# Kernel tuning notes

Measured on AMD Instinct MI355X. Metric: run time of the kernel, lower is better.

The kernel has to match this reference:

```python
import jax, jax.numpy as jnp
import numpy as np

EMB_SIZE = 768
BLOCK_SIZE = 64
OFFSET = 1  # bert cls offset


def setup_inputs() -> dict:
    key = jax.random.key(0)
    ks = jax.random.split(key, 10)
    n, c, d, h, E, M, P = 4, 1024, 768, 12, 42, 8, 1024
    sequence_output = jax.random.normal(ks[0], (n, c, d), jnp.float32)
    attention = jax.random.uniform(ks[1], (n, h, c, c), jnp.float32)
    attention = attention / attention.sum(-1, keepdims=True)  # softmax-like rows
    Wh = jax.random.normal(ks[2], (EMB_SIZE, 2 * d), jnp.float32) * 0.02
    bh = jax.random.normal(ks[3], (EMB_SIZE,), jnp.float32) * 0.02
    Wt = jax.random.normal(ks[4], (EMB_SIZE, 2 * d), jnp.float32) * 0.02
    bt = jax.random.normal(ks[5], (EMB_SIZE,), jnp.float32) * 0.02
    Wb = jax.random.normal(ks[6], (99, EMB_SIZE * BLOCK_SIZE), jnp.float32) * 0.02
    mention_pos = jax.random.randint(ks[7], (n, E, M), 0, c - 1 - OFFSET, jnp.int32)
    mention_mask = jax.random.randint(ks[8], (n, E, M), 0, 2, jnp.int32)
    mention_mask = mention_mask.at[:, :, 0].set(1)  # every entity has >=1 mention
    hts = jax.random.randint(ks[9], (n, P, 2), 0, E, jnp.int32)
    return {"sequence_output": sequence_output, "attention": attention,
            "Wh": Wh, "bh": bh, "Wt": Wt, "bt": bt, "Wb": Wb,
            "mention_pos": mention_pos, "mention_mask": mention_mask, "hts": hts}


def _get_hrt_doc(seq, att, pos, mask, ht):
    # seq [c,d], att [h,c,c], pos/mask [E,M], ht [P,2]
    p = pos + OFFSET                                   # [E,M]
    valid = mask > 0
    memb = seq[p]                                      # [E,M,d] gather
    e_emb = jax.scipy.special.logsumexp(
        jnp.where(valid[..., None], memb, -jnp.inf), axis=1)  # [E,d]
    matt = att[:, p]                                   # [h,E,M,c] gather
    cnt = valid.sum(1).astype(seq.dtype)               # [E]
    e_att = (matt * valid[None, :, :, None].astype(seq.dtype)).sum(2)
    e_att = jnp.transpose(e_att, (1, 0, 2)) / cnt[:, None, None]  # [E,h,c] mention mean
    hs = e_emb[ht[:, 0]]                               # [P,d]
    ts = e_emb[ht[:, 1]]
    h_att = e_att[ht[:, 0]]                            # [P,h,c]
    t_att = e_att[ht[:, 1]]
    ht_att = (h_att * t_att).mean(1)                   # [P,c] head mean
    ht_att = ht_att / (ht_att.sum(1, keepdims=True) + 1e-5)
    rs = jnp.einsum('ld,rl->rd', seq, ht_att)          # [P,d]
    return hs, ts, rs


def reference(sequence_output, attention, Wh, bh, Wt, bt, Wb,
              mention_pos, mention_mask, hts):
    d = sequence_output.shape[-1]
    hs, ts, rs = jax.vmap(_get_hrt_doc)(sequence_output, attention,
                                        mention_pos, mention_mask, hts)
    hs = hs.reshape(-1, d)
    ts = ts.reshape(-1, d)
    rs = rs.reshape(-1, d)
    hs = jnp.tanh(jnp.concatenate([hs, rs], axis=1) @ Wh.T + bh)
    ts = jnp.tanh(jnp.concatenate([ts, rs], axis=1) @ Wt.T + bt)
    nb = EMB_SIZE // BLOCK_SIZE
    b1 = hs.reshape(-1, nb, BLOCK_SIZE)
    b2 = ts.reshape(-1, nb, BLOCK_SIZE)
    bl = (b1[:, :, :, None] * b2[:, :, None, :]).reshape(-1, EMB_SIZE * BLOCK_SIZE)
    logits = bl @ Wb.T                                 # [N, num_labels+2]
    return logits
```

## Files before the change

### kernel.cpp

```cpp
#include <hip/hip_runtime.h>
#include <hip/hip_bf16.h>
#include <hip/hip_fp16.h>
#include <math.h>

#define NDOC 4
#define CCC  1024
#define DDD  768
#define HHH  12
#define EEE  42
#define MMM  8
#define PPP  1024
#define NBQ  12
#define NK   99
#define NPAD 112

typedef __attribute__((ext_vector_type(8))) short short8v;
typedef __attribute__((ext_vector_type(8))) _Float16 half8;
typedef __attribute__((ext_vector_type(4))) float floatx4;

__device__ __forceinline__ unsigned short f32_to_bf16u(float f) {
  return __builtin_bit_cast(unsigned short, __float2bfloat16(f));
}
__device__ __forceinline__ unsigned short f32_to_f16u(float f) {
  return __builtin_bit_cast(unsigned short, __float2half(f));
}

__global__ __launch_bounds__(256) void k_eemb(const float* __restrict__ seq,
    const int* __restrict__ pos, const int* __restrict__ mask,
    unsigned short* __restrict__ eembB) {
  int e = blockIdx.x, doc = blockIdx.y;
  int base = (doc*EEE + e)*MMM;
  int p[MMM], mk[MMM];
#pragma unroll
  for (int m = 0; m < MMM; ++m) { p[m] = pos[base+m] + 1; mk[m] = mask[base+m]; }
  for (int d0 = threadIdx.x; d0 < DDD; d0 += 256) {
    float v[MMM]; float mx = -INFINITY;
#pragma unroll
    for (int m = 0; m < MMM; ++m) {
      v[m] = seq[(doc*CCC + p[m])*DDD + d0];
      if (mk[m]) mx = fmaxf(mx, v[m]);
    }
    float s = 0.f;
#pragma unroll
    for (int m = 0; m < MMM; ++m) if (mk[m]) s += expf(v[m]-mx);
    eembB[(doc*EEE + e)*DDD + d0] = f32_to_bf16u(logf(s) + mx);
  }
}

__global__ __launch_bounds__(256) void k_eatt(const float* __restrict__ att,
    const int* __restrict__ pos, const int* __restrict__ mask,
    float* __restrict__ eatt) {
  int head = blockIdx.x, e = blockIdx.y, doc = blockIdx.z;
  int base = (doc*EEE + e)*MMM;
  int j = threadIdx.x * 4;
  float ax=0.f, ay=0.f, az=0.f, aw=0.f; float cnt = 0.f;
#pragma unroll
  for (int m = 0; m < MMM; ++m) {
    int mk = mask[base+m];
    cnt += (float)mk;
    if (mk) {
      int pp = pos[base+m] + 1;
      const float4 a = *(const float4*)&att[((size_t)(doc*HHH + head)*CCC + pp)*CCC + j];
      ax += a.x; ay += a.y; az += a.z; aw += a.w;
    }
  }
  float inv = 1.f / cnt;
  float4 o; o.x = ax*inv; o.y = ay*inv; o.z = az*inv; o.w = aw*inv;
  *(float4*)&eatt[((size_t)((doc*EEE + e)*HHH + head))*CCC + j] = o;
}

__global__ __launch_bounds__(256) void k_htatt(const float* __restrict__ eatt,
    const int* __restrict__ hts, unsigned short* __restrict__ htB) {
  int b = blockIdx.x; int doc = b >> 10; int r = b & 1023;
  int h0 = hts[(doc*PPP + r)*2 + 0];
  int t0 = hts[(doc*PPP + r)*2 + 1];
  const float* ea0 = &eatt[(size_t)((doc*EEE + h0)*HHH)*CCC];
  const float* ea1 = &eatt[(size_t)((doc*EEE + t0)*HHH)*CCC];
  int j = threadIdx.x * 4;
  float vx=0.f, vy=0.f, vz=0.f, vw=0.f;
#pragma unroll
  for (int hh = 0; hh < HHH; ++hh) {
    const float4 a  = *(const float4*)&ea0[hh*CCC + j];
    const float4 bq = *(const float4*)&ea1[hh*CCC + j];
    vx += a.x*bq.x; vy += a.y*bq.y; vz += a.z*bq.z; vw += a.w*bq.w;
  }
  const float inv12 = 1.f/12.f;
  vx *= inv12; vy *= inv12; vz *= inv12; vw *= inv12;
  float part = vx + vy + vz + vw;
  __shared__ float red[4];
  for (int off = 32; off > 0; off >>= 1) part += __shfl_down(part, off, 64);
  int lane = threadIdx.x & 63, wv = threadIdx.x >> 6;
  if (lane == 0) red[wv] = part;
  __syncthreads();
  if (threadIdx.x == 0) red[0] = red[0]+red[1]+red[2]+red[3];
  __syncthreads();
  float sc = 1.f / (red[0] + 1e-5f);
  unsigned short o[4];
  o[0] = f32_to_bf16u(vx*sc); o[1] = f32_to_bf16u(vy*sc);
  o[2] = f32_to_bf16u(vz*sc); o[3] = f32_to_bf16u(vw*sc);
  *(uint2*)&htB[((size_t)(doc*PPP + r))*CCC + j] = *(const uint2*)o;
}

__global__ __launch_bounds__(256) void k_packW(const float* __restrict__ Wh,
    const float* __restrict__ Wt, unsigned short* __restrict__ WB) {
  int gid = blockIdx.x*256 + threadIdx.x;
  int half = gid >= 147456;
  int loc = half ? gid - 147456 : gid;
  const float* src = (half ? Wt : Wh) + (size_t)loc*8;
  float4 v0 = *(const float4*)src;
  float4 v1 = *(const float4*)(src+4);
  unsigned short o[8];
  o[0]=f32_to_bf16u(v0.x); o[1]=f32_to_bf16u(v0.y); o[2]=f32_to_bf16u(v0.z); o[3]=f32_to_bf16u(v0.w);
  o[4]=f32_to_bf16u(v1.x); o[5]=f32_to_bf16u(v1.y); o[6]=f32_to_bf16u(v1.z); o[7]=f32_to_bf16u(v1.w);
  *(uint4*)&WB[(size_t)half*1179648 + (size_t)loc*8] = *(const uint4*)o;
}

__global__ __launch_bounds__(256) void k_seqT(const float* __restrict__ seq,
    unsigned short* __restrict__ seqTB) {
  __shared__ float tl[64][65];
  int d0 = blockIdx.x * 64, c0 = blockIdx.y * 64, doc = blockIdx.z;
  int t = threadIdx.x;
#pragma unroll
  for (int rep = 0; rep < 4; ++rep) {
    int cr = rep*16 + (t >> 4);
    int d4 = (t & 15) * 4;
    float4 v = *(const float4*)&seq[((size_t)doc*CCC + c0 + cr)*DDD + d0 + d4];
    tl[cr][d4+0]=v.x; tl[cr][d4+1]=v.y; tl[cr][d4+2]=v.z; tl[cr][d4+3]=v.w;
  }
  __syncthreads();
#pragma unroll
  for (int rep = 0; rep < 4; ++rep) {
    int dr = rep*16 + (t >> 4);
    int c4 = (t & 15) * 4;
    unsigned short o[4];
#pragma unroll
    for (int kq = 0; kq < 4; ++kq)
      o[kq] = f32_to_bf16u(tl[c4+kq][dr]);
    *(uint2*)&seqTB[((size_t)doc*DDD + d0 + dr)*CCC + c0 + c4] = *(const uint2*)o;
  }
}

__global__ __launch_bounds__(256) void k_rs_mfma(
    const unsigned short* __restrict__ htB,
    const unsigned short* __restrict__ seqTB,
    unsigned short* __restrict__ rsB) {
  __shared__ unsigned short A_l[4096];
  __shared__ unsigned short B_l[4096];
  const int n0 = blockIdx.x * 128;
  const int m0 = blockIdx.y * 128;
  const int doc = m0 >> 10;
  const int mloc = m0 & 1023;
  const int t = threadIdx.x;
  const int lane = t & 63;
  const int ln = lane & 15, q4 = lane >> 4;
  const int w = t >> 6;
  const int wr = w >> 1, wc = w & 1;

  const int r0 = t >> 2;
  const int koff = (t & 3) * 8;
  const unsigned short* srcA0 = htB + ((size_t)doc*CCC + mloc + r0)*CCC + koff;
  const unsigned short* srcA1 = htB + ((size_t)doc*CCC + mloc + r0 + 64)*CCC + koff;
  const unsigned short* srcB0 = seqTB + ((size_t)doc*DDD + n0 + r0)*CCC + koff;
  const unsigned short* srcB1 = seqTB + ((size_t)doc*DDD + n0 + r0 + 64)*CCC + koff;

  floatx4 acc[4][4];
#pragma unroll
  for (int i = 0; i < 4; ++i)
#pragma unroll
    for (int j = 0; j < 4; ++j) acc[i][j] = (floatx4){0.f,0.f,0.f,0.f};

  for (int k0 = 0; k0 < CCC; k0 += 32) {
    uint4 va0 = *(const uint4*)(srcA0 + k0);
    uint4 va1 = *(const uint4*)(srcA1 + k0);
    uint4 vb0 = *(const uint4*)(srcB0 + k0);
    uint4 vb1 = *(const uint4*)(srcB1 + k0);
    __syncthreads();
    *(uint4*)&A_l[(size_t)t*8]       = va0;
    *(uint4*)&A_l[(size_t)(t+256)*8] = va1;
    *(uint4*)&B_l[(size_t)t*8]       = vb0;
    *(uint4*)&B_l[(size_t)(t+256)*8] = vb1;
    __syncthreads();
    short8v a[4], b[4];
#pragma unroll
    for (int rt = 0; rt < 4; ++rt)
      a[rt] = *(const short8v*)&A_l[((wr*64 + rt*16 + ln)*4 + q4)*8];
#pragma unroll
    for (int nt = 0; nt < 4; ++nt)
      b[nt] = *(const short8v*)&B_l[((wc*64 + nt*16 + ln)*4 + q4)*8];
#pragma unroll
    for (int rt = 0; rt < 4; ++rt)
#pragma unroll
      for (int nt = 0; nt < 4; ++nt)
        acc[rt][nt] = __builtin_amdgcn_mfma_f32_16x16x32_bf16(a[rt], b[nt], acc[rt][nt], 0, 0, 0);
  }
#pragma unroll
  for (int rt = 0; rt < 4; ++rt)
#pragma unroll
    for (int nt = 0; nt < 4; ++nt) {
      int col = n0 + wc*64 + nt*16 + ln;
#pragma unroll
      for (int reg = 0; reg < 4; ++reg) {
        int row = m0 + wr*64 + rt*16 + q4*4 + reg;
        rsB[(size_t)row*DDD + col] = f32_to_bf16u(acc[rt][nt][reg]);
      }
    }
}

__global__ __launch_bounds__(256) void k_heads_mfma(
    const unsigned short* __restrict__ eembB,
    const unsigned short* __restrict__ rsB,
    const int* __restrict__ hts,
    const unsigned short* __restrict__ WB,
    const float* __restrict__ bh, const float* __restrict__ bt,
    float* __restrict__ hsb, float* __restrict__ tsb) {
  __shared__ unsigned short A_l[4096];
  __shared__ unsigned short B_l[4096];
  const int which = blockIdx.z;
  const int n0 = blockIdx.x * 128;
  const int m0 = blockIdx.y * 128;
  const int doc = m0 >> 10;
  const int t = threadIdx.x;
  const int lane = t & 63;
  const int ln = lane & 15, q4 = lane >> 4;
  const int w = t >> 6;
  const int wr = w >> 1, wc = w & 1;

  const int r0 = t >> 2;
  const int koff = (t & 3) * 8;
  const int rgA0 = m0 + r0, rgA1 = m0 + r0 + 64;
  const int idx0 = hts[rgA0*2 + which];
  const int idx1 = hts[rgA1*2 + which];
  const unsigned short* srcE0 = eembB + (size_t)(doc*EEE + idx0)*DDD + koff;
  const unsigned short* srcE1 = eembB + (size_t)(doc*EEE + idx1)*DDD + koff;
  const unsigned short* srcR0 = rsB + (size_t)rgA0*DDD + koff;
  const unsigned short* srcR1 = rsB + (size_t)rgA1*DDD + koff;
  const unsigned short* WBz = WB + (size_t)which*1179648;
  const unsigned short* srcW0 = WBz + (size_t)(n0 + r0)*1536 + koff;
  const unsigned short* srcW1 = WBz + (size_t)(n0 + r0 + 64)*1536 + koff;

  floatx4 acc[4][4];
#pragma unroll
  for (int i = 0; i < 4; ++i)
#pragma unroll
    for (int j = 0; j < 4; ++j) acc[i][j] = (floatx4){0.f,0.f,0.f,0.f};

  for (int k0 = 0; k0 < 1536; k0 += 32) {
    uint4 va0 = (k0 < DDD) ? *(const uint4*)(srcE0 + k0) : *(const uint4*)(srcR0 + (k0 - DDD));
    uint4 va1 = (k0 < DDD) ? *(const uint4*)(srcE1 + k0) : *(const uint4*)(srcR1 + (k0 - DDD));
    uint4 vb0 = *(const uint4*)(srcW0 + k0);
    uint4 vb1 = *(const uint4*)(srcW1 + k0);
    __syncthreads();
    *(uint4*)&A_l[(size_t)t*8]       = va0;
    *(uint4*)&A_l[(size_t)(t+256)*8] = va1;
    *(uint4*)&B_l[(size_t)t*8]       = vb0;
    *(uint4*)&B_l[(size_t)(t+256)*8] = vb1;
    __syncthreads();
    short8v a[4], b[4];
#pragma unroll
    for (int rt = 0; rt < 4; ++rt)
      a[rt] = *(const short8v*)&A_l[((wr*64 + rt*16 + ln)*4 + q4)*8];
#pragma unroll
    for (int nt = 0; nt < 4; ++nt)
      b[nt] = *(const short8v*)&B_l[((wc*64 + nt*16 + ln)*4 + q4)*8];
#pragma unroll
    for (int rt = 0; rt < 4; ++rt)
#pragma unroll
      for (int nt = 0; nt < 4; ++nt)
        acc[rt][nt] = __builtin_amdgcn_mfma_f32_16x16x32_bf16(a[rt], b[nt], acc[rt][nt], 0, 0, 0);
  }
  const float* bias = which ? bt : bh;
  float* outp = which ? tsb : hsb;
#pragma unroll
  for (int rt = 0; rt < 4; ++rt)
#pragma unroll
    for (int nt = 0; nt < 4; ++nt) {
      int col = n0 + wc*64 + nt*16 + ln;
      float bsv = bias[col];
#pragma unroll
      for (int reg = 0; reg < 4; ++reg) {
        int row = m0 + wr*64 + rt*16 + q4*4 + reg;
        outp[(size_t)row*DDD + col] = tanhf(acc[rt][nt][reg] + bsv);
      }
    }
}

__global__ __launch_bounds__(256) void k_prep_w(const float* __restrict__ Wb,
    unsigned short* __restrict__ Wp) {
  int t = blockIdx.x*256 + threadIdx.x;
  int j = (t & 7) * 8;
  int n = (t >> 3) % NPAD;
  int ki = t / 896;
  unsigned short o[8];
  if (n < NK) {
    const float* src = &Wb[(size_t)n*49152 + ki*64 + j];
    float4 v0 = *(const float4*)src;
    float4 v1 = *(const float4*)(src+4);
    o[0]=f32_to_f16u(v0.x); o[1]=f32_to_f16u(v0.y); o[2]=f32_to_f16u(v0.z); o[3]=f32_to_f16u(v0.w);
    o[4]=f32_to_f16u(v1.x); o[5]=f32_to_f16u(v1.y); o[6]=f32_to_f16u(v1.z); o[7]=f32_to_f16u(v1.w);
  } else {
#pragma unroll
    for (int e=0;e<8;++e) o[e]=0;
  }
  *(uint4*)&Wp[(size_t)ki*7168 + n*64 + j] = *(const uint4*)o;
}

__global__ __launch_bounds__(256) void k_pack_hs(const float* __restrict__ hs,
    unsigned short* __restrict__ hsT) {
  __shared__ float tl[64][65];
  int i0 = blockIdx.x * 64, r0 = blockIdx.y * 64;
  int t = threadIdx.x;
#pragma unroll
  for (int rep = 0; rep < 4; ++rep) {
    int r = rep*16 + (t >> 4);
    int c4 = (t & 15) * 4;
    float4 v = *(const float4*)&hs[(size_t)(r0 + r)*DDD + i0 + c4];
    tl[r][c4+0]=v.x; tl[r][c4+1]=v.y; tl[r][c4+2]=v.z; tl[r][c4+3]=v.w;
  }
  __syncthreads();
#pragma unroll
  for (int rep = 0; rep < 4; ++rep) {
    int i = rep*16 + (t >> 4);
    int r4 = (t & 15) * 4;
    unsigned short o[4];
#pragma unroll
    for (int kq = 0; kq < 4; ++kq)
      o[kq] = f32_to_f16u(tl[r4+kq][i]);
    *(uint2*)&hsT[(size_t)(i0 + i)*4096 + r0 + r4] = *(const uint2*)o;
  }
}

__global__ __launch_bounds__(256, 3) void k_logits_mfma(
    const unsigned short* __restrict__ hsT,
    const float* __restrict__ tsb,
    const unsigned short* __restrict__ Wp,
    unsigned short* __restrict__ P) {
  __shared__ unsigned short hsT_l[32*128];
  __shared__ unsigned short Bt_l[2*NPAD*72];
  const int slice = blockIdx.x;
  const int kbase = (slice >> 1)*64 + (slice & 1)*32;
  const int mtile = blockIdx.y;
  const int t = threadIdx.x;
  const int w = t >> 6;
  const int lane = t & 63;
  const int ln = lane & 15;
  const int q = lane >> 4;
  const int m0w = mtile*128 + w*32;

#pragma unroll
  for (int rep = 0; rep < 2; ++rep) {
    int c16 = t + rep*256;
    int ii = c16 >> 4;
    int c8 = (c16 & 15) * 8;
    uint4 v = *(const uint4*)&hsT[(size_t)(kbase + ii)*4096 + mtile*128 + c8];
    *(uint4*)&hsT_l[ii*128 + c8] = v;
  }

  __half2 tsr2[2][2][4];
#pragma unroll
  for (int rt = 0; rt < 2; ++rt) {
    int row = m0w + rt*16 + ln;
    int nb = kbase >> 6;
#pragma unroll
    for (int js = 0; js < 2; ++js) {
      const float* p = &tsb[(size_t)row*DDD + nb*64 + js*32 + q*8];
      float4 v0 = *(const float4*)p;
      float4 v1 = *(const float4*)(p+4);
      tsr2[rt][js][0] = __floats2half2_rn(v0.x, v0.y);
      tsr2[rt][js][1] = __floats2half2_rn(v0.z, v0.w);
      tsr2[rt][js][2] = __floats2half2_rn(v1.x, v1.y);
      tsr2[rt][js][3] = __floats2half2_rn(v1.z, v1.w);
    }
  }

  floatx4 acc[2][7];
#pragma unroll
  for (int rt = 0; rt < 2; ++rt)
#pragma unroll
    for (int nt = 0; nt < 7; ++nt)
      acc[rt][nt] = (floatx4){0.f,0.f,0.f,0.f};

  uint4 wreg[4];
#pragma unroll
  for (int r = 0; r < 4; ++r) {
    int chunk = t + r*256;
    if (chunk < 896) wreg[r] = *(const uint4*)&Wp[(size_t)kbase*7168 + chunk*8];
  }
#pragma unroll
  for (int r = 0; r < 4; ++r) {
    int chunk = t + r*256;
    if (chunk < 896) {
      int n = chunk >> 3, j8 = (chunk & 7)*8;
      *(uint4*)&Bt_l[n*72 + j8] = wreg[r];
    }
  }
  __syncthreads();

  for (int ii = 0; ii < 32; ++ii) {
    const unsigned short* bufc = Bt_l + (ii & 1)*(NPAD*72);
    if (ii < 31) {
      int ki = kbase + ii + 1;
#pragma unroll
      for (int r = 0; r < 4; ++r) {
        int chunk = t + r*256;
        if (chunk < 896) wreg[r] = *(const uint4*)&Wp[(size_t)ki*7168 + chunk*8];
      }
    }
    __half2 hh[2];
#pragma unroll
    for (int rt = 0; rt < 2; ++rt) {
      unsigned short hb = hsT_l[ii*128 + w*32 + rt*16 + ln];
      hh[rt] = __half2half2(__ushort_as_half(hb));
    }
#pragma unroll
    for (int js = 0; js < 2; ++js) {
      half8 a[2];
#pragma unroll
      for (int rt = 0; rt < 2; ++rt) {
        uint4 au;
        au.x = __builtin_bit_cast(unsigned int, __hmul2(hh[rt], tsr2[rt][js][0]));
        au.y = __builtin_bit_cast(unsigned int, __hmul2(hh[rt], tsr2[rt][js][1]));
        au.z = __builtin_bit_cast(unsigned int, __hmul2(hh[rt], tsr2[rt][js][2]));
        au.w = __builtin_bit_cast(unsigned int, __hmul2(hh[rt], tsr2[rt][js][3]));
        a[rt] = __builtin_bit_cast(half8, au);
      }
#pragma unroll
      for (int nt = 0; nt < 7; ++nt) {
        half8 b = __builtin_bit_cast(half8,
            *(const short8v*)&bufc[(nt*16 + ln)*72 + js*32 + q*8]);
#pragma unroll
        for (int rt = 0; rt < 2; ++rt)
          acc[rt][nt] = __builtin_amdgcn_mfma_f32_16x16x32_f16(a[rt], b, acc[rt][nt], 0, 0, 0);
      }
    }
    if (ii < 31) {
      __syncthreads();
#pragma unroll
      for (int r = 0; r < 4; ++r) {
        int chunk = t + r*256;
        if (chunk < 896) {
          int n = chunk >> 3, j8 = (chunk & 7)*8;
          *(uint4*)&Bt_l[((ii+1) & 1)*(NPAD*72) + n*72 + j8] = wreg[r];
        }
      }
      __syncthreads();
    }
  }

  unsigned short* Ps = P + (size_t)slice*(4096*NPAD);
#pragma unroll
  for (int nt = 0; nt < 7; ++nt) {
    int col = nt*16 + ln;
#pragma unroll
    for (int rt = 0; rt < 2; ++rt) {
#pragma unroll
      for (int reg = 0; reg < 4; ++reg) {
        int row = m0w + rt*16 + q*4 + reg;
        Ps[(size_t)row*NPAD + col] = f32_to_f16u(acc[rt][nt][reg]);
      }
    }
  }
}

__global__ __launch_bounds__(256) void k_logred(const unsigned short* __restrict__ P,
    float* __restrict__ out) {
  int idx = blockIdx.x*256 + threadIdx.x;
  int r = idx / NPAD;
  int c = idx % NPAD;
  if (c >= NK) return;
  float s = 0.f;
#pragma unroll
  for (int sl = 0; sl < 24; ++sl)
    s += __half2float(__ushort_as_half(P[(size_t)sl*(4096*NPAD) + idx]));
  out[(size_t)r*NK + c] = s;
}

extern "C" void kernel_launch(void* const* d_in, const int* in_sizes, int n_in,
                              void* d_out, int out_size, void* d_ws, size_t ws_size,
                              hipStream_t stream) {
  const float* seq  = (const float*)d_in[0];
  const float* att  = (const float*)d_in[1];
  const float* Wh   = (const float*)d_in[2];
  const float* bh   = (const float*)d_in[3];
  const float* Wt   = (const float*)d_in[4];
  const float* bt   = (const float*)d_in[5];
  const float* Wb   = (const float*)d_in[6];
  const int* pos    = (const int*)d_in[7];
  const int* mask   = (const int*)d_in[8];
  const int* hts    = (const int*)d_in[9];
  float* out = (float*)d_out;

  float* ws = (float*)d_ws;
  float*          eatt  = ws;
  unsigned short* htB   = (unsigned short*)(ws + 2064384);
  unsigned short* eembB = (unsigned short*)(ws + 4161536);
  unsigned short* seqTB = (unsigned short*)(ws + 4226048);
  unsigned short* WhtB  = (unsigned short*)(ws + 5798912);
  unsigned short* rsB   = (unsigned short*)(ws + 6978560);
  float*          hsb   = ws + 8551424;
  float*          tsb   = ws + 11697152;
  unsigned short* WpB   = (unsigned short*)eatt;
  unsigned short* hsTB  = (unsigned short*)seqTB;
  unsigned short* Pp    = (unsigned short*)(ws + 5798912);

  k_eemb<<<dim3(EEE, NDOC), 256, 0, stream>>>(seq, pos, mask, eembB);
  k_eatt<<<dim3(HHH, EEE, NDOC), 256, 0, stream>>>(att, pos, mask, eatt);
  k_htatt<<<dim3(NDOC*PPP), 256, 0, stream>>>(eatt, hts, htB);
  k_packW<<<dim3(1152), 256, 0, stream>>>(Wh, Wt, WhtB);
  k_seqT<<<dim3(DDD/64, CCC/64, NDOC), 256, 0, stream>>>(seq, seqTB);
  k_rs_mfma<<<dim3(6, 32), 256, 0, stream>>>(htB, seqTB, rsB);
  k_prep_w<<<dim3(2688), 256, 0, stream>>>(Wb, WpB);
  k_heads_mfma<<<dim3(6, 32, 2), 256, 0, stream>>>(eembB, rsB, hts, WhtB, bh, bt, hsb, tsb);
  k_pack_hs<<<dim3(DDD/64, 4096/64), 256, 0, stream>>>(hsb, hsTB);
  k_logits_mfma<<<dim3(24, 32), 256, 0, stream>>>(hsTB, tsb, WpB, Pp);
  k_logred<<<dim3(4096*NPAD/256), 256, 0, stream>>>(Pp, out);
}
```

Before: 226.5 us.

## Pre-swizzle Wb into MFMA fragment order and double per-warp row tile in logits kernel

The Wb prep kernel now writes fp16 weights in the exact lane order of the MFMA B-fragment, so the logits kernel can copy them linearly into LDS and read each fragment with a contiguous lane*8 load instead of a padded strided layout. The logits kernel also drops to 128 threads per block, with each warp covering 64 rows (4 row tiles) instead of 32, so each B fragment feeds twice as many MFMAs. This cuts LDS traffic and address math per MFMA, at the cost of more accumulator registers per thread and fewer warps per block to hide latency.

```diff
diff --git a/kernel.cpp b/kernel.cpp
--- a/kernel.cpp
+++ b/kernel.cpp
@@ -287,12 +287,12 @@
 __global__ __launch_bounds__(256) void k_prep_w(const float* __restrict__ Wb,
     unsigned short* __restrict__ Wp) {
   int t = blockIdx.x*256 + threadIdx.x;
-  int j = (t & 7) * 8;
+  int j8 = (t & 7) * 8;
   int n = (t >> 3) % NPAD;
   int ki = t / 896;
   unsigned short o[8];
   if (n < NK) {
-    const float* src = &Wb[(size_t)n*49152 + ki*64 + j];
+    const float* src = &Wb[(size_t)n*49152 + ki*64 + j8];
     float4 v0 = *(const float4*)src;
     float4 v1 = *(const float4*)(src+4);
     o[0]=f32_to_f16u(v0.x); o[1]=f32_to_f16u(v0.y); o[2]=f32_to_f16u(v0.z); o[3]=f32_to_f16u(v0.w);
@@ -301,7 +301,10 @@
 #pragma unroll
     for (int e=0;e<8;++e) o[e]=0;
   }
-  *(uint4*)&Wp[(size_t)ki*7168 + n*64 + j] = *(const uint4*)o;
+  int js = (t & 7) >> 2, q = t & 3;
+  int nt = n >> 4, lnn = n & 15;
+  int c = ((js*7 + nt)*4 + q)*16 + lnn;
+  *(uint4*)&Wp[(size_t)ki*7168 + c*8] = *(const uint4*)o;
 }
 
 __global__ __launch_bounds__(256) void k_pack_hs(const float* __restrict__ hs,
@@ -329,13 +332,13 @@
   }
 }
 
-__global__ __launch_bounds__(256, 3) void k_logits_mfma(
+__global__ __launch_bounds__(128, 2) void k_logits_mfma(
     const unsigned short* __restrict__ hsT,
     const float* __restrict__ tsb,
     const unsigned short* __restrict__ Wp,
     unsigned short* __restrict__ P) {
   __shared__ unsigned short hsT_l[32*128];
-  __shared__ unsigned short Bt_l[2*NPAD*72];
+  __shared__ unsigned short Bt_l[2*7168];
   const int slice = blockIdx.x;
   const int kbase = (slice >> 1)*64 + (slice & 1)*32;
   const int mtile = blockIdx.y;
@@ -344,78 +347,71 @@
   const int lane = t & 63;
   const int ln = lane & 15;
   const int q = lane >> 4;
-  const int m0w = mtile*128 + w*32;
-
-#pragma unroll
-  for (int rep = 0; rep < 2; ++rep) {
-    int c16 = t + rep*256;
+  const int m0w = mtile*128 + w*64;
+
+#pragma unroll
+  for (int rep = 0; rep < 4; ++rep) {
+    int c16 = t + rep*128;
     int ii = c16 >> 4;
     int c8 = (c16 & 15) * 8;
     uint4 v = *(const uint4*)&hsT[(size_t)(kbase + ii)*4096 + mtile*128 + c8];
     *(uint4*)&hsT_l[ii*128 + c8] = v;
   }
 
-  __half2 tsr2[2][2][4];
-#pragma unroll
-  for (int rt = 0; rt < 2; ++rt) {
-    int row = m0w + rt*16 + ln;
+  __half2 tsr2[4][2][4];
+  {
     int nb = kbase >> 6;
 #pragma unroll
-    for (int js = 0; js < 2; ++js) {
-      const float* p = &tsb[(size_t)row*DDD + nb*64 + js*32 + q*8];
-      float4 v0 = *(const float4*)p;
-      float4 v1 = *(const float4*)(p+4);
-      tsr2[rt][js][0] = __floats2half2_rn(v0.x, v0.y);
-      tsr2[rt][js][1] = __floats2half2_rn(v0.z, v0.w);
-      tsr2[rt][js][2] = __floats2half2_rn(v1.x, v1.y);
-      tsr2[rt][js][3] = __floats2half2_rn(v1.z, v1.w);
-    }
-  }
-
-  floatx4 acc[2][7];
-#pragma unroll
-  for (int rt = 0; rt < 2; ++rt)
+    for (int rt = 0; rt < 4; ++rt) {
+      int row = m0w + rt*16 + ln;
+#pragma unroll
+      for (int js = 0; js < 2; ++js) {
+        const float* p = &tsb[(size_t)row*DDD + nb*64 + js*32 + q*8];
+        float4 v0 = *(const float4*)p;
+        float4 v1 = *(const float4*)(p+4);
+        tsr2[rt][js][0] = __floats2half2_rn(v0.x, v0.y);
+        tsr2[rt][js][1] = __floats2half2_rn(v0.z, v0.w);
+        tsr2[rt][js][2] = __floats2half2_rn(v1.x, v1.y);
+        tsr2[rt][js][3] = __floats2half2_rn(v1.z, v1.w);
+      }
+    }
+  }
+
+  floatx4 acc[4][7];
+#pragma unroll
+  for (int rt = 0; rt < 4; ++rt)
 #pragma unroll
     for (int nt = 0; nt < 7; ++nt)
       acc[rt][nt] = (floatx4){0.f,0.f,0.f,0.f};
 
-  uint4 wreg[4];
-#pragma unroll
-  for (int r = 0; r < 4; ++r) {
-    int chunk = t + r*256;
-    if (chunk < 896) wreg[r] = *(const uint4*)&Wp[(size_t)kbase*7168 + chunk*8];
-  }
-#pragma unroll
-  for (int r = 0; r < 4; ++r) {
-    int chunk = t + r*256;
-    if (chunk < 896) {
-      int n = chunk >> 3, j8 = (chunk & 7)*8;
-      *(uint4*)&Bt_l[n*72 + j8] = wreg[r];
-    }
-  }
+  uint4 wreg[7];
+#pragma unroll
+  for (int r = 0; r < 7; ++r)
+    wreg[r] = *(const uint4*)&Wp[(size_t)kbase*7168 + (t + r*128)*8];
+#pragma unroll
+  for (int r = 0; r < 7; ++r)
+    *(uint4*)&Bt_l[(t + r*128)*8] = wreg[r];
   __syncthreads();
 
   for (int ii = 0; ii < 32; ++ii) {
-    const unsigned short* bufc = Bt_l + (ii & 1)*(NPAD*72);
+    const unsigned short* bufc = Bt_l + (ii & 1)*7168;
     if (ii < 31) {
       int ki = kbase + ii + 1;
 #pragma unroll
-      for (int r = 0; r < 4; ++r) {
-        int chunk = t + r*256;
-        if (chunk < 896) wreg[r] = *(const uint4*)&Wp[(size_t)ki*7168 + chunk*8];
-      }
-    }
-    __half2 hh[2];
-#pragma unroll
-    for (int rt = 0; rt < 2; ++rt) {
-      unsigned short hb = hsT_l[ii*128 + w*32 + rt*16 + ln];
+      for (int r = 0; r < 7; ++r)
+        wreg[r] = *(const uint4*)&Wp[(size_t)ki*7168 + (t + r*128)*8];
+    }
+    __half2 hh[4];
+#pragma unroll
+    for (int rt = 0; rt < 4; ++rt) {
+      unsigned short hb = hsT_l[ii*128 + w*64 + rt*16 + ln];
       hh[rt] = __half2half2(__ushort_as_half(hb));
     }
 #pragma unroll
     for (int js = 0; js < 2; ++js) {
-      half8 a[2];
-#pragma unroll
-      for (int rt = 0; rt < 2; ++rt) {
+      half8 a[4];
+#pragma unroll
+      for (int rt = 0; rt < 4; ++rt) {
         uint4 au;
         au.x = __builtin_bit_cast(unsigned int, __hmul2(hh[rt], tsr2[rt][js][0]));
         au.y = __builtin_bit_cast(unsigned int, __hmul2(hh[rt], tsr2[rt][js][1]));
@@ -426,22 +422,17 @@
 #pragma unroll
       for (int nt = 0; nt < 7; ++nt) {
         half8 b = __builtin_bit_cast(half8,
-            *(const short8v*)&bufc[(nt*16 + ln)*72 + js*32 + q*8]);
-#pragma unroll
-        for (int rt = 0; rt < 2; ++rt)
+            *(const short8v*)&bufc[((js*7 + nt)*4)*128 + lane*8]);
+#pragma unroll
+        for (int rt = 0; rt < 4; ++rt)
           acc[rt][nt] = __builtin_amdgcn_mfma_f32_16x16x32_f16(a[rt], b, acc[rt][nt], 0, 0, 0);
       }
     }
     if (ii < 31) {
       __syncthreads();
 #pragma unroll
-      for (int r = 0; r < 4; ++r) {
-        int chunk = t + r*256;
-        if (chunk < 896) {
-          int n = chunk >> 3, j8 = (chunk & 7)*8;
-          *(uint4*)&Bt_l[((ii+1) & 1)*(NPAD*72) + n*72 + j8] = wreg[r];
-        }
-      }
+      for (int r = 0; r < 7; ++r)
+        *(uint4*)&Bt_l[((ii+1) & 1)*7168 + (t + r*128)*8] = wreg[r];
       __syncthreads();
     }
   }
@@ -451,7 +442,7 @@
   for (int nt = 0; nt < 7; ++nt) {
     int col = nt*16 + ln;
 #pragma unroll
-    for (int rt = 0; rt < 2; ++rt) {
+    for (int rt = 0; rt < 4; ++rt) {
 #pragma unroll
       for (int reg = 0; reg < 4; ++reg) {
         int row = m0w + rt*16 + q*4 + reg;
@@ -511,6 +502,6 @@
   k_prep_w<<<dim3(2688), 256, 0, stream>>>(Wb, WpB);
   k_heads_mfma<<<dim3(6, 32, 2), 256, 0, stream>>>(eembB, rsB, hts, WhtB, bh, bt, hsb, tsb);
   k_pack_hs<<<dim3(DDD/64, 4096/64), 256, 0, stream>>>(hsb, hsTB);
-  k_logits_mfma<<<dim3(24, 32), 256, 0, stream>>>(hsTB, tsb, WpB, Pp);
+  k_logits_mfma<<<dim3(24, 32), 128, 0, stream>>>(hsTB, tsb, WpB, Pp);
   k_logred<<<dim3(4096*NPAD/256), 256, 0, stream>>>(Pp, out);
 }
```

Measured after the change: 221.8 us. 1.02x faster.
